# Kernel tuning notes

Hardware: AMD Instinct MI355X
Metric: run time of the kernel (lower is better)

Reference implementation:

```python
import jax, jax.numpy as jnp
import numpy as np

B, S, D = 4, 2048, 1024
H, HD = 16, 64
MLP = 4 * D
EPS = 1e-6


def _rms_norm(x, scale):
    var = jnp.mean(jnp.square(x), axis=-1, keepdims=True)
    return x * jax.lax.rsqrt(var + EPS) * scale


def setup_inputs() -> dict:
    key = jax.random.key(0)
    ks = jax.random.split(key, 8)
    sd = D ** -0.5
    return {
        "x": jax.random.normal(ks[0], (B, S, D), jnp.float32),
        "pre_norm_scale": jnp.ones((D,), jnp.float32),
        "w_mlp_in": jax.random.normal(ks[1], (D, MLP), jnp.float32) * sd,   # MLPBlockInput, no bias
        "wq": jax.random.normal(ks[2], (D, H, HD), jnp.float32) * sd,
        "wk": jax.random.normal(ks[3], (D, H, HD), jnp.float32) * sd,
        "wv": jax.random.normal(ks[4], (D, H, HD), jnp.float32) * sd,
        "w_mlp_out": jax.random.normal(ks[5], (MLP, D), jnp.float32) * (MLP ** -0.5),
        "b_mlp_out": jnp.zeros((D,), jnp.float32),
        "w_attn_out": jax.random.normal(ks[6], (H, HD, D), jnp.float32) * sd,  # DenseGeneral axis=(-2,-1)
        "b_attn_out": jnp.zeros((D,), jnp.float32),
    }


def reference(x, pre_norm_scale, w_mlp_in, wq, wk, wv, w_mlp_out, b_mlp_out,
              w_attn_out, b_attn_out):
    residual = x
    xn = _rms_norm(x, pre_norm_scale)                      # pre_norm (TPNorm)

    # QKVMLPDense: fused MLP-input + QKV projections
    h = jax.nn.gelu(jnp.einsum("bsd,df->bsf", xn, w_mlp_in))   # [B,S,MLP]
    q = jnp.einsum("bsd,dhk->bshk", xn, wq)                    # [B,S,H,HD]
    k = jnp.einsum("bsd,dhk->bshk", xn, wk)
    v = jnp.einsum("bsd,dhk->bshk", xn, wv)

    # dot_product_attention (mask=None)
    scores = jnp.einsum("bqhd,bkhd->bhqk", q, k) / jnp.sqrt(jnp.asarray(HD, x.dtype))
    probs = jax.nn.softmax(scores, axis=-1)
    attn_v = jnp.einsum("bhqk,bkhd->bqhd", probs, v)           # [B,S,H,HD]

    # AttnMLPOut: mlp_out + attn_out
    mlp_out = jnp.einsum("bsf,fd->bsd", h, w_mlp_out) + b_mlp_out
    attn_out = jnp.einsum("bqhk,hkd->bqd", attn_v, w_attn_out) + b_attn_out
    block_out = mlp_out + attn_out                              # dropout is identity (train=False)
    return residual + block_out
```

## Files before the change

### kernel.cpp

```cpp
#include <hip/hip_runtime.h>
#include <cstdint>
#include <cstddef>

typedef float floatx4 __attribute__((ext_vector_type(4)));
typedef short bf16x8 __attribute__((ext_vector_type(8)));

#define MFMA(a, b, c) __builtin_amdgcn_mfma_f32_16x16x32_bf16((a), (b), (c), 0, 0, 0)

__device__ __forceinline__ unsigned short f2bf(float f) {
  union { float f; unsigned int u; } v; v.f = f;
  unsigned int u = v.u;
  unsigned int r = (u + 0x7FFFu + ((u >> 16) & 1u)) >> 16;
  return (unsigned short)r;
}

__device__ __forceinline__ void gload_lds16(const unsigned short* g, unsigned short* s) {
  __builtin_amdgcn_global_load_lds(
      (const __attribute__((address_space(1))) unsigned int*)g,
      (__attribute__((address_space(3))) unsigned int*)s, 16, 0, 0);
}

__device__ __forceinline__ float gelu_f(float v) {
  float z = 0.7978845608028654f * (v + 0.044715f * v * v * v);
  float e = __expf(2.0f * z);
  float th = 1.0f - 2.0f / (e + 1.0f);
  return 0.5f * v * (1.0f + th);
}

__global__ __launch_bounds__(256) void prep_all(
    const float* __restrict__ w_mlp_in, const float* __restrict__ wq,
    const float* __restrict__ wk, const float* __restrict__ wv,
    const float* __restrict__ w_mlp_out, const float* __restrict__ w_attn_out,
    const float* __restrict__ x, const float* __restrict__ pns,
    unsigned short* __restrict__ wcatT, unsigned short* __restrict__ wcat2T,
    unsigned short* __restrict__ xn) {
  __shared__ float tile[32][33];
  __shared__ float ws4[4];
  int id = blockIdx.x;
  if (id >= 12288) {
    int row = id - 12288;
    const float4 v = ((const float4*)(x + (size_t)row * 1024))[threadIdx.x];
    float ss = v.x * v.x + v.y * v.y + v.z * v.z + v.w * v.w;
#pragma unroll
    for (int off = 1; off < 64; off <<= 1) ss += __shfl_xor(ss, off, 64);
    if ((threadIdx.x & 63) == 0) ws4[threadIdx.x >> 6] = ss;
    __syncthreads();
    float tot = ws4[0] + ws4[1] + ws4[2] + ws4[3];
    float rs = rsqrtf(tot * (1.0f / 1024.0f) + 1e-6f);
    const float4 sc = ((const float4*)pns)[threadIdx.x];
    uint2 o;
    o.x = (unsigned)f2bf(v.x * rs * sc.x) | ((unsigned)f2bf(v.y * rs * sc.y) << 16);
    o.y = (unsigned)f2bf(v.z * rs * sc.z) | ((unsigned)f2bf(v.w * rs * sc.w) << 16);
    ((uint2*)(xn + (size_t)row * 1024))[threadIdx.x] = o;
    return;
  }
  const float* src; unsigned short* dst; int C, ldd, bx, by, q;
  if (id < 4096)       { src = w_mlp_in;   dst = wcatT;                        C = 4096; ldd = 1024; q = id;         bx = q & 127; by = q >> 7; }
  else if (id < 5120)  { src = wq;         dst = wcatT + (size_t)4096 * 1024;  C = 1024; ldd = 1024; q = id - 4096;  bx = q & 31;  by = q >> 5; }
  else if (id < 6144)  { src = wk;         dst = wcatT + (size_t)5120 * 1024;  C = 1024; ldd = 1024; q = id - 5120;  bx = q & 31;  by = q >> 5; }
  else if (id < 7168)  { src = wv;         dst = wcatT + (size_t)6144 * 1024;  C = 1024; ldd = 1024; q = id - 6144;  bx = q & 31;  by = q >> 5; }
  else if (id < 11264) { src = w_mlp_out;  dst = wcat2T;                       C = 1024; ldd = 5120; q = id - 7168;  bx = q & 31;  by = q >> 5; }
  else                 { src = w_attn_out; dst = wcat2T + 4096;                C = 1024; ldd = 5120; q = id - 11264; bx = q & 31;  by = q >> 5; }
  int tx = threadIdx.x & 31, ty = threadIdx.x >> 5;
#pragma unroll
  for (int i = 0; i < 4; i++) {
    int r = ty + i * 8;
    tile[r][tx] = src[(size_t)(by * 32 + r) * C + bx * 32 + tx];
  }
  __syncthreads();
#pragma unroll
  for (int i = 0; i < 4; i++) {
    int r = ty + i * 8;
    dst[(size_t)(bx * 32 + r) * ldd + by * 32 + tx] = f2bf(tile[tx][r]);
  }
}

template <int MODE>
__global__ __launch_bounds__(256, 2) void gemm_bt(
    const unsigned short* __restrict__ A, const unsigned short* __restrict__ BT,
    int K, void* __restrict__ outp,
    const float* __restrict__ bias1, const float* __restrict__ bias2,
    const float* __restrict__ resid,
    int msplit, int tm, int tn,
    unsigned short* __restrict__ q_out, unsigned short* __restrict__ k_out,
    unsigned short* __restrict__ v_out) {
  __shared__ unsigned short As[2][128 * 32];
  __shared__ unsigned short Bs[2][128 * 32];

  int id = blockIdx.x + gridDim.x * blockIdx.y;
  int xcd = id & 7, j = id >> 3;
  int mh = xcd % msplit, nq = xcd / msplit;
  int by = mh * tm + j / tn;
  int bx = nq * tn + j % tn;
  int m0 = by * 128, n0 = bx * 128;

  int t = threadIdx.x, lane = t & 63, wave = t >> 6;
  int l15 = lane & 15, quad = lane >> 4;
  int wm = (wave & 1) * 64, wn = (wave >> 1) * 64;

  floatx4 acc[4][4] = {};

  int lr = lane >> 2;
  int lg = (lane & 3) ^ ((lane >> 3) & 3);
  int ch0 = wave * 2, ch1 = wave * 2 + 1;
  const unsigned short* gA0 = A + (size_t)(m0 + ch0 * 16 + lr) * K + lg * 8;
  const unsigned short* gA1 = A + (size_t)(m0 + ch1 * 16 + lr) * K + lg * 8;
  const unsigned short* gB0 = BT + (size_t)(n0 + ch0 * 16 + lr) * K + lg * 8;
  const unsigned short* gB1 = BT + (size_t)(n0 + ch1 * 16 + lr) * K + lg * 8;
  unsigned short* sA0[2] = {&As[0][ch0 * 512 + lane * 8], &As[1][ch0 * 512 + lane * 8]};
  unsigned short* sA1[2] = {&As[0][ch1 * 512 + lane * 8], &As[1][ch1 * 512 + lane * 8]};
  unsigned short* sB0[2] = {&Bs[0][ch0 * 512 + lane * 8], &Bs[1][ch0 * 512 + lane * 8]};
  unsigned short* sB1[2] = {&Bs[0][ch1 * 512 + lane * 8], &Bs[1][ch1 * 512 + lane * 8]};

  int fo = (4 * l15 + (quad ^ ((l15 >> 1) & 3))) * 8;
  int ca = (wm >> 4);
  int cb = (wn >> 4);

  for (int kt = 0; kt < K; kt += 64) {
    __syncthreads();
#pragma unroll
    for (int kk = 0; kk < 2; kk++) {
      int kg = kt + kk * 32;
      gload_lds16(gA0 + kg, sA0[kk]);
      gload_lds16(gA1 + kg, sA1[kk]);
      gload_lds16(gB0 + kg, sB0[kk]);
      gload_lds16(gB1 + kg, sB1[kk]);
    }
    __syncthreads();
#pragma unroll
    for (int kk = 0; kk < 2; kk++) {
      bf16x8 a[4], b[4];
#pragma unroll
      for (int im = 0; im < 4; im++)
        a[im] = *(const bf16x8*)&As[kk][(ca + im) * 512 + fo];
#pragma unroll
      for (int in_ = 0; in_ < 4; in_++)
        b[in_] = *(const bf16x8*)&Bs[kk][(cb + in_) * 512 + fo];
#pragma unroll
      for (int im = 0; im < 4; im++)
#pragma unroll
        for (int in_ = 0; in_ < 4; in_++)
          acc[im][in_] = MFMA(a[im], b[in_], acc[im][in_]);
    }
  }

#pragma unroll
  for (int im = 0; im < 4; im++) {
#pragma unroll
    for (int in_ = 0; in_ < 4; in_++) {
      int row0 = m0 + wm + im * 16 + quad * 4;
      int col = n0 + wn + in_ * 16 + l15;
      if constexpr (MODE == 6) {
        if (n0 < 4096) {
#pragma unroll
          for (int r = 0; r < 4; r++) {
            __builtin_nontemporal_store(f2bf(gelu_f(acc[im][in_][r])),
                &((unsigned short*)outp)[(size_t)(row0 + r) * 5120 + col]);
          }
        } else {
          int seg = (n0 - 4096) >> 10;
          int cs = col - 4096 - (seg << 10);
          int h = cs >> 6, hd = cs & 63;
          int b_ = row0 >> 11, s0 = row0 & 2047;
          if (seg == 2) {
            unsigned long long o =
                (unsigned long long)((unsigned)f2bf(acc[im][in_][0]) |
                                     ((unsigned)f2bf(acc[im][in_][1]) << 16)) |
                ((unsigned long long)((unsigned)f2bf(acc[im][in_][2]) |
                                      ((unsigned)f2bf(acc[im][in_][3]) << 16)) << 32);
            __builtin_nontemporal_store(o,
                (unsigned long long*)&v_out[(((size_t)(b_ * 16 + h)) * 64 + hd) * 2048 + s0]);
          } else {
            float sc = (seg == 0) ? 0.125f : 1.0f;
            unsigned short* dst = (seg == 0) ? q_out : k_out;
#pragma unroll
            for (int r = 0; r < 4; r++) {
              __builtin_nontemporal_store(f2bf(acc[im][in_][r] * sc),
                  &dst[(((size_t)(b_ * 16 + h)) * 2048 + s0 + r) * 64 + hd]);
            }
          }
        }
      } else {
        float bsum = bias1[col] + bias2[col];
#pragma unroll
        for (int r = 0; r < 4; r++) {
          size_t idx = (size_t)(row0 + r) * 1024 + col;
          float res = __builtin_nontemporal_load(&resid[idx]);
          __builtin_nontemporal_store(acc[im][in_][r] + bsum + res, &((float*)outp)[idx]);
        }
      }
    }
  }
}

__global__ __launch_bounds__(256, 3) void flash_attn(
    const unsigned short* __restrict__ q_buf, const unsigned short* __restrict__ k_buf,
    const unsigned short* __restrict__ v_buf, unsigned short* __restrict__ cat) {
  constexpr int S = 2048, HD = 64;
  constexpr int LK = 68, LV = 68, LP = 68;
  __shared__ unsigned short Ks[2][64 * LK];
  __shared__ unsigned short Vs[2][64 * LV];
  __shared__ unsigned short Ps[4][32 * LP];

  int id = blockIdx.x + gridDim.x * blockIdx.y;
  int xcd = id & 7, j = id >> 3;
  int bh = xcd * 8 + (j >> 4);
  int qbk = j & 15;

  int t = threadIdx.x, lane = t & 63, wave = t >> 6;
  int l15 = lane & 15, quad = lane >> 4;

  const unsigned short* qp = q_buf + (size_t)bh * S * HD;
  const unsigned short* kp = k_buf + (size_t)bh * S * HD;
  const unsigned short* vp = v_buf + (size_t)bh * HD * S;

  int q0 = qbk * 128 + wave * 32;
  bf16x8 aQ[2][2];
#pragma unroll
  for (int qf = 0; qf < 2; qf++) {
    aQ[qf][0] = *(const bf16x8*)&qp[(size_t)(q0 + qf * 16 + l15) * HD + quad * 8];
    aQ[qf][1] = *(const bf16x8*)&qp[(size_t)(q0 + qf * 16 + l15) * HD + 32 + quad * 8];
  }

  floatx4 acc_o[2][4] = {};
  float lrow[2][4] = {};

  int kr = t >> 3, kc = (t & 7) * 8;

  uint4 rK0 = *(const uint4*)&kp[(size_t)kr * HD + kc];
  uint4 rK1 = *(const uint4*)&kp[(size_t)(kr + 32) * HD + kc];
  uint4 rV0 = *(const uint4*)&vp[(size_t)kr * S + kc];
  uint4 rV1 = *(const uint4*)&vp[(size_t)(kr + 32) * S + kc];
  *(uint4*)&Ks[0][kr * LK + kc] = rK0;
  *(uint4*)&Ks[0][(kr + 32) * LK + kc] = rK1;
  *(uint4*)&Vs[0][kr * LV + kc] = rV0;
  *(uint4*)&Vs[0][(kr + 32) * LV + kc] = rV1;
  rK0 = *(const uint4*)&kp[(size_t)(64 + kr) * HD + kc];
  rK1 = *(const uint4*)&kp[(size_t)(64 + kr + 32) * HD + kc];
  rV0 = *(const uint4*)&vp[(size_t)kr * S + 64 + kc];
  rV1 = *(const uint4*)&vp[(size_t)(kr + 32) * S + 64 + kc];
  asm volatile("s_waitcnt lgkmcnt(0)" ::: "memory");
  __builtin_amdgcn_s_barrier();
  __builtin_amdgcn_sched_barrier(0);

  for (int kv = 0; kv < S; kv += 64) {
    int cur = (kv >> 6) & 1;
    if (kv + 64 < S) {
      *(uint4*)&Ks[cur ^ 1][kr * LK + kc] = rK0;
      *(uint4*)&Ks[cur ^ 1][(kr + 32) * LK + kc] = rK1;
      *(uint4*)&Vs[cur ^ 1][kr * LV + kc] = rV0;
      *(uint4*)&Vs[cur ^ 1][(kr + 32) * LV + kc] = rV1;
    }

    floatx4 z[2][4];
#pragma unroll
    for (int cg = 0; cg < 4; cg++) {
      bf16x8 bk0 = *(const bf16x8*)&Ks[cur][(cg * 16 + l15) * LK + quad * 8];
      bf16x8 bk1 = *(const bf16x8*)&Ks[cur][(cg * 16 + l15) * LK + 32 + quad * 8];
#pragma unroll
      for (int qf = 0; qf < 2; qf++) {
        floatx4 acc = {};
        acc = MFMA(aQ[qf][0], bk0, acc);
        acc = MFMA(aQ[qf][1], bk1, acc);
        z[qf][cg] = acc;
      }
    }
    if (kv + 128 < S) {
      rK0 = *(const uint4*)&kp[(size_t)(kv + 128 + kr) * HD + kc];
      rK1 = *(const uint4*)&kp[(size_t)(kv + 128 + kr + 32) * HD + kc];
      rV0 = *(const uint4*)&vp[(size_t)kr * S + kv + 128 + kc];
      rV1 = *(const uint4*)&vp[(size_t)(kr + 32) * S + kv + 128 + kc];
    }
#pragma unroll
    for (int qf = 0; qf < 2; qf++)
#pragma unroll
      for (int cg = 0; cg < 4; cg++)
#pragma unroll
        for (int r = 0; r < 4; r++) {
          float e = __expf(z[qf][cg][r]);
          lrow[qf][r] += e;
          Ps[wave][(qf * 16 + quad * 4 + r) * LP + cg * 16 + l15] = f2bf(e);
        }
    asm volatile("s_waitcnt lgkmcnt(0)" ::: "memory");
#pragma unroll
    for (int c = 0; c < 2; c++) {
      bf16x8 aP[2];
#pragma unroll
      for (int qf = 0; qf < 2; qf++) {
        const unsigned short* pp = &Ps[wave][(qf * 16 + l15) * LP + c * 32 + quad * 8];
        ((uint2*)&aP[qf])[0] = *(const uint2*)pp;
        ((uint2*)&aP[qf])[1] = *(const uint2*)(pp + 4);
      }
#pragma unroll
      for (int n = 0; n < 4; n++) {
        bf16x8 bv = *(const bf16x8*)&Vs[cur][(n * 16 + l15) * LV + c * 32 + quad * 8];
        acc_o[0][n] = MFMA(aP[0], bv, acc_o[0][n]);
        acc_o[1][n] = MFMA(aP[1], bv, acc_o[1][n]);
      }
    }
    asm volatile("s_waitcnt lgkmcnt(0)" ::: "memory");
    __builtin_amdgcn_s_barrier();
    __builtin_amdgcn_sched_barrier(0);
  }

#pragma unroll
  for (int qf = 0; qf < 2; qf++)
#pragma unroll
    for (int r = 0; r < 4; r++) {
      float s = lrow[qf][r];
#pragma unroll
      for (int off = 1; off < 16; off <<= 1) s += __shfl_xor(s, off, 16);
      lrow[qf][r] = s;
    }

  int b_ = bh >> 4, h = bh & 15;
#pragma unroll
  for (int qf = 0; qf < 2; qf++)
#pragma unroll
    for (int r = 0; r < 4; r++) {
      float inv = 1.0f / lrow[qf][r];
      int srow = q0 + qf * 16 + quad * 4 + r;
      size_t base = ((size_t)(b_ * 2048 + srow)) * 5120 + 4096 + h * 64;
#pragma unroll
      for (int n = 0; n < 4; n++)
        __builtin_nontemporal_store(f2bf(acc_o[qf][n][r] * inv),
                                    &cat[base + n * 16 + l15]);
    }
}

extern "C" void kernel_launch(void* const* d_in, const int* in_sizes, int n_in,
                              void* d_out, int out_size, void* d_ws, size_t ws_size,
                              hipStream_t stream) {
  (void)in_sizes; (void)n_in; (void)out_size; (void)ws_size;
  const float* x          = (const float*)d_in[0];
  const float* pns        = (const float*)d_in[1];
  const float* w_mlp_in   = (const float*)d_in[2];
  const float* wq         = (const float*)d_in[3];
  const float* wk         = (const float*)d_in[4];
  const float* wv         = (const float*)d_in[5];
  const float* w_mlp_out  = (const float*)d_in[6];
  const float* b_mlp_out  = (const float*)d_in[7];
  const float* w_attn_out = (const float*)d_in[8];
  const float* b_attn_out = (const float*)d_in[9];
  float* out = (float*)d_out;

  char* ws = (char*)d_ws;
  size_t off = 0;
  auto alloc = [&](size_t bytes) {
    void* p = ws + off;
    off += (bytes + 255) & ~(size_t)255;
    return p;
  };
  const size_t M = 8192;
  unsigned short* xn     = (unsigned short*)alloc(M * 1024 * 2);
  unsigned short* wcatT  = (unsigned short*)alloc((size_t)7168 * 1024 * 2);
  unsigned short* wcat2T = (unsigned short*)alloc((size_t)1024 * 5120 * 2);
  unsigned short* cat    = (unsigned short*)alloc(M * 5120 * 2);
  unsigned short* qb     = (unsigned short*)alloc(M * 1024 * 2);
  unsigned short* kb     = (unsigned short*)alloc(M * 1024 * 2);
  unsigned short* vb     = (unsigned short*)alloc(M * 1024 * 2);

  prep_all<<<dim3(20480), 256, 0, stream>>>(
      w_mlp_in, wq, wk, wv, w_mlp_out, w_attn_out, x, pns, wcatT, wcat2T, xn);

  gemm_bt<6><<<dim3(56, 64), 256, 0, stream>>>(
      xn, wcatT, 1024, cat, nullptr, nullptr, nullptr, 2, 32, 14, qb, kb, vb);

  flash_attn<<<dim3(16, 64), 256, 0, stream>>>(qb, kb, vb, cat);

  gemm_bt<7><<<dim3(8, 64), 256, 0, stream>>>(
      cat, wcat2T, 5120, out, b_mlp_out, b_attn_out, x, 2, 32, 2, nullptr, nullptr, nullptr);
}
```

Before: 546.7 us.

## Single-buffer K/V LDS tiles in flash attention with two barriers per step

Replaces the double-buffered K/V shared-memory tiles with single buffers bracketed by two __syncthreads per iteration. The next tile is prefetched into registers right after the store instead of after QK^T. It also lowers the launch bound to two blocks per SM, widens the K/V row padding from 68 to 72, and turns the output stores into ordinary stores. This uses less LDS and a simpler schedule, at the cost of an extra barrier each iteration and less overlap between loads and compute.

```diff
diff --git a/kernel.cpp b/kernel.cpp
--- a/kernel.cpp
+++ b/kernel.cpp
@@ -193,13 +193,13 @@
   }
 }
 
-__global__ __launch_bounds__(256, 3) void flash_attn(
+__global__ __launch_bounds__(256, 2) void flash_attn(
     const unsigned short* __restrict__ q_buf, const unsigned short* __restrict__ k_buf,
     const unsigned short* __restrict__ v_buf, unsigned short* __restrict__ cat) {
   constexpr int S = 2048, HD = 64;
-  constexpr int LK = 68, LV = 68, LP = 68;
-  __shared__ unsigned short Ks[2][64 * LK];
-  __shared__ unsigned short Vs[2][64 * LV];
+  constexpr int LK = 72, LV = 72, LP = 68;
+  __shared__ unsigned short Ks[64 * LK];
+  __shared__ unsigned short Vs[64 * LV];
   __shared__ unsigned short Ps[4][32 * LP];
 
   int id = blockIdx.x + gridDim.x * blockIdx.y;
@@ -231,32 +231,26 @@
   uint4 rK1 = *(const uint4*)&kp[(size_t)(kr + 32) * HD + kc];
   uint4 rV0 = *(const uint4*)&vp[(size_t)kr * S + kc];
   uint4 rV1 = *(const uint4*)&vp[(size_t)(kr + 32) * S + kc];
-  *(uint4*)&Ks[0][kr * LK + kc] = rK0;
-  *(uint4*)&Ks[0][(kr + 32) * LK + kc] = rK1;
-  *(uint4*)&Vs[0][kr * LV + kc] = rV0;
-  *(uint4*)&Vs[0][(kr + 32) * LV + kc] = rV1;
-  rK0 = *(const uint4*)&kp[(size_t)(64 + kr) * HD + kc];
-  rK1 = *(const uint4*)&kp[(size_t)(64 + kr + 32) * HD + kc];
-  rV0 = *(const uint4*)&vp[(size_t)kr * S + 64 + kc];
-  rV1 = *(const uint4*)&vp[(size_t)(kr + 32) * S + 64 + kc];
-  asm volatile("s_waitcnt lgkmcnt(0)" ::: "memory");
-  __builtin_amdgcn_s_barrier();
-  __builtin_amdgcn_sched_barrier(0);
 
   for (int kv = 0; kv < S; kv += 64) {
-    int cur = (kv >> 6) & 1;
+    __syncthreads();
+    *(uint4*)&Ks[kr * LK + kc] = rK0;
+    *(uint4*)&Ks[(kr + 32) * LK + kc] = rK1;
+    *(uint4*)&Vs[kr * LV + kc] = rV0;
+    *(uint4*)&Vs[(kr + 32) * LV + kc] = rV1;
+    __syncthreads();
     if (kv + 64 < S) {
-      *(uint4*)&Ks[cur ^ 1][kr * LK + kc] = rK0;
-      *(uint4*)&Ks[cur ^ 1][(kr + 32) * LK + kc] = rK1;
-      *(uint4*)&Vs[cur ^ 1][kr * LV + kc] = rV0;
-      *(uint4*)&Vs[cur ^ 1][(kr + 32) * LV + kc] = rV1;
+      rK0 = *(const uint4*)&kp[(size_t)(kv + 64 + kr) * HD + kc];
+      rK1 = *(const uint4*)&kp[(size_t)(kv + 64 + kr + 32) * HD + kc];
+      rV0 = *(const uint4*)&vp[(size_t)kr * S + kv + 64 + kc];
+      rV1 = *(const uint4*)&vp[(size_t)(kr + 32) * S + kv + 64 + kc];
     }
 
     floatx4 z[2][4];
 #pragma unroll
     for (int cg = 0; cg < 4; cg++) {
-      bf16x8 bk0 = *(const bf16x8*)&Ks[cur][(cg * 16 + l15) * LK + quad * 8];
-      bf16x8 bk1 = *(const bf16x8*)&Ks[cur][(cg * 16 + l15) * LK + 32 + quad * 8];
+      bf16x8 bk0 = *(const bf16x8*)&Ks[(cg * 16 + l15) * LK + quad * 8];
+      bf16x8 bk1 = *(const bf16x8*)&Ks[(cg * 16 + l15) * LK + 32 + quad * 8];
 #pragma unroll
       for (int qf = 0; qf < 2; qf++) {
         floatx4 acc = {};
@@ -265,12 +259,6 @@
         z[qf][cg] = acc;
       }
     }
-    if (kv + 128 < S) {
-      rK0 = *(const uint4*)&kp[(size_t)(kv + 128 + kr) * HD + kc];
-      rK1 = *(const uint4*)&kp[(size_t)(kv + 128 + kr + 32) * HD + kc];
-      rV0 = *(const uint4*)&vp[(size_t)kr * S + kv + 128 + kc];
-      rV1 = *(const uint4*)&vp[(size_t)(kr + 32) * S + kv + 128 + kc];
-    }
 #pragma unroll
     for (int qf = 0; qf < 2; qf++)
 #pragma unroll
@@ -293,14 +281,11 @@
       }
 #pragma unroll
       for (int n = 0; n < 4; n++) {
-        bf16x8 bv = *(const bf16x8*)&Vs[cur][(n * 16 + l15) * LV + c * 32 + quad * 8];
+        bf16x8 bv = *(const bf16x8*)&Vs[(n * 16 + l15) * LV + c * 32 + quad * 8];
         acc_o[0][n] = MFMA(aP[0], bv, acc_o[0][n]);
         acc_o[1][n] = MFMA(aP[1], bv, acc_o[1][n]);
       }
     }
-    asm volatile("s_waitcnt lgkmcnt(0)" ::: "memory");
-    __builtin_amdgcn_s_barrier();
-    __builtin_amdgcn_sched_barrier(0);
   }
 
 #pragma unroll
@@ -323,8 +308,7 @@
       size_t base = ((size_t)(b_ * 2048 + srow)) * 5120 + 4096 + h * 64;
 #pragma unroll
       for (int n = 0; n < 4; n++)
-        __builtin_nontemporal_store(f2bf(acc_o[qf][n][r] * inv),
-                                    &cat[base + n * 16 + l15]);
+        cat[base + n * 16 + l15] = f2bf(acc_o[qf][n][r] * inv);
     }
 }
 
```

Result: faster. 520.7 us (-4.8%).
